# Optimization experiments

Hardware: AMD Instinct MI355X
Metric: run time of the kernel (lower is better)

## Reference

```python
import jax, jax.numpy as jnp
import numpy as np

D_MODEL = 1024
N_HEADS = 16
D_K = D_MODEL // N_HEADS


def setup_inputs() -> dict:
    key = jax.random.key(0)
    kx, kq, kk, kv, ko = jax.random.split(key, 5)
    scale = 1.0 / np.sqrt(D_MODEL)
    return {
        "x": jax.random.normal(kx, (2, 2048, D_MODEL), dtype=jnp.float32),
        "W_Q": jax.random.normal(kq, (D_MODEL, D_MODEL), dtype=jnp.float32) * scale,
        "W_K": jax.random.normal(kk, (D_MODEL, D_MODEL), dtype=jnp.float32) * scale,
        "W_V": jax.random.normal(kv, (D_MODEL, D_MODEL), dtype=jnp.float32) * scale,
        "W_O": jax.random.normal(ko, (D_MODEL, D_MODEL), dtype=jnp.float32) * scale,
    }


def reference(x, W_Q, W_K, W_V, W_O) -> jnp.ndarray:
    B, S, _ = x.shape
    # Projections; weights stored as (d_model, d_model), applied as x @ W (Linear weight transposed convention folded into init)
    def heads(w):
        return jnp.einsum('bsd,de->bse', x, w).reshape(B, S, N_HEADS, D_K).transpose(0, 2, 1, 3)
    Q, K, V = heads(W_Q), heads(W_K), heads(W_V)  # (B,H,S,d_k)
    scores = jnp.einsum('bhqd,bhkd->bhqk', Q, K) / jnp.sqrt(jnp.asarray(D_K, x.dtype))
    causal_mask = jnp.triu(jnp.ones((S, S), dtype=bool), k=1)  # True above diagonal
    scores = jnp.where(causal_mask[None, None], jnp.asarray(-jnp.inf, x.dtype), scores)
    attn = jax.nn.softmax(scores, axis=-1)
    out = jnp.einsum('bhqk,bhkd->bhqd', attn, V)  # (B,H,S,d_k)
    out = out.transpose(0, 2, 1, 3).reshape(B, S, N_HEADS * D_K)
    return jnp.einsum('bsd,de->bse', out, W_O)
```

## Files before the change

### kernel.cpp

```cpp
#include <hip/hip_runtime.h>

typedef unsigned short u16;
typedef unsigned int u32;
typedef __attribute__((ext_vector_type(8))) __bf16 bf16x8;
typedef __attribute__((ext_vector_type(2))) __bf16 bf16x2;
typedef __attribute__((ext_vector_type(4))) float f32x4;
typedef __attribute__((ext_vector_type(16))) float f32x16;
typedef __attribute__((ext_vector_type(4))) u32 u32x4;

__device__ inline u16 f2bf(float f) {
  unsigned u = __builtin_bit_cast(unsigned, f);
  u += 0x7FFFu + ((u >> 16) & 1u);
  return (u16)(u >> 16);
}

__device__ inline u32 packbf(float a, float b) {
  bf16x2 t;
  t[0] = (__bf16)a;
  t[1] = (__bf16)b;
  return __builtin_bit_cast(u32, t);
}

__device__ inline void async16(const void* g, void* l) {
  __builtin_amdgcn_global_load_lds((const __attribute__((address_space(1))) void*)g,
                                   (__attribute__((address_space(3))) void*)l, 16, 0, 0);
}

__global__ __launch_bounds__(256) void xconv(const float* __restrict__ x, u16* __restrict__ xb) {
  int i = blockIdx.x * 256 + threadIdx.x;
  float4 v = ((const float4*)x)[i];
  ushort4 r;
  r.x = f2bf(v.x); r.y = f2bf(v.y); r.z = f2bf(v.z); r.w = f2bf(v.w);
  ((ushort4*)xb)[i] = r;
}

__global__ __launch_bounds__(256) void wtrans4(const float* __restrict__ W0,
                                               const float* __restrict__ W1,
                                               const float* __restrict__ W2,
                                               const float* __restrict__ W3,
                                               u16* __restrict__ WtQKV,
                                               u16* __restrict__ WtO) {
  __shared__ u16 tile[32][33];
  const int z = blockIdx.z;
  const float* W = (z == 0) ? W0 : (z == 1) ? W1 : (z == 2) ? W2 : W3;
  u16* Wt = (z < 3) ? (WtQKV + (size_t)z * 1024 * 1024) : WtO;
  const float s = (z == 0) ? 0.18033688011112042f : 1.0f;
  const int e0 = blockIdx.x * 32;
  const int d0 = blockIdx.y * 32;
  const int tx = threadIdx.x & 31;
  const int ty = threadIdx.x >> 5;
#pragma unroll
  for (int i = ty; i < 32; i += 8)
    tile[i][tx] = f2bf(W[(size_t)(d0 + i) * 1024 + e0 + tx] * s);
  __syncthreads();
#pragma unroll
  for (int i = ty; i < 32; i += 8)
    Wt[(size_t)(e0 + i) * 1024 + d0 + tx] = tile[tx][i];
}

__global__ __launch_bounds__(256) void vtrans(const u16* __restrict__ QKV, u16* __restrict__ Vtg) {
  __shared__ u16 t[32][66];
  const int tid = threadIdx.x;
  const int s0 = blockIdx.x * 32, dg0 = blockIdx.y * 64, b = blockIdx.z;
  {
    const int i = tid >> 3, c = (tid & 7) * 8;
    uint4 v = *(const uint4*)(QKV + (size_t)(b * 2048 + s0 + i) * 3072 + 2048 + dg0 + c);
    u16 tmp[8];
    *(uint4*)tmp = v;
#pragma unroll
    for (int e = 0; e < 8; ++e) t[i][c + e] = tmp[e];
  }
  __syncthreads();
  {
    const int r = tid >> 2, cg = (tid & 3) * 8;
    u16 tmp[8];
#pragma unroll
    for (int e = 0; e < 8; ++e) tmp[e] = t[cg + e][r];
    *(uint4*)(Vtg + (size_t)(b * 1024 + dg0 + r) * 2048 + s0 + cg) = *(uint4*)tmp;
  }
}

template <int OUT_BF16>
__global__ __launch_bounds__(256) void gemm_bt(const u16* __restrict__ A,
                                               const u16* __restrict__ Bt,
                                               void* __restrict__ Cp,
                                               int M, int N, int K) {
  __shared__ __align__(16) u16 As[128 * 32];
  __shared__ __align__(16) u16 Bs[128 * 32];
  const int tid = threadIdx.x;
  const int lane = tid & 63;
  const int wave = tid >> 6;
  const int lr = lane & 15;
  const int lk = (lane >> 4) * 8;
  const int wm = (wave >> 1) * 64;
  const int wn = (wave & 1) * 64;
  const int bm = blockIdx.x * 128;
  const int bn = blockIdx.y * 128;
  const int srow = lane >> 2;
  const int scol = (lane & 3) * 8;

  f32x4 acc[4][4] = {};

  for (int k0 = 0; k0 < K; k0 += 32) {
#pragma unroll
    for (int r = 0; r < 2; ++r) {
      const int chunk = r * 4 + wave;
      const int row = chunk * 16 + srow;
      async16(A + (size_t)(bm + row) * K + k0 + scol, &As[chunk * 512 + lane * 8]);
      async16(Bt + (size_t)(bn + row) * K + k0 + scol, &Bs[chunk * 512 + lane * 8]);
    }
    __syncthreads();
    bf16x8 a[4], b[4];
#pragma unroll
    for (int i = 0; i < 4; ++i) {
      a[i] = *(const bf16x8*)&As[(wm + i * 16 + lr) * 32 + lk];
      b[i] = *(const bf16x8*)&Bs[(wn + i * 16 + lr) * 32 + lk];
    }
#pragma unroll
    for (int mi = 0; mi < 4; ++mi)
#pragma unroll
      for (int ni = 0; ni < 4; ++ni)
        acc[mi][ni] = __builtin_amdgcn_mfma_f32_16x16x32_bf16(a[mi], b[ni], acc[mi][ni], 0, 0, 0);
    __syncthreads();
  }

#pragma unroll
  for (int mi = 0; mi < 4; ++mi) {
#pragma unroll
    for (int ni = 0; ni < 4; ++ni) {
      const int col = bn + wn + ni * 16 + lr;
#pragma unroll
      for (int j = 0; j < 4; ++j) {
        const int row = bm + wm + mi * 16 + (lane >> 4) * 4 + j;
        if (OUT_BF16)
          ((u16*)Cp)[(size_t)row * N + col] = f2bf(acc[mi][ni][j]);
        else
          ((float*)Cp)[(size_t)row * N + col] = acc[mi][ni][j];
      }
    }
  }
}

__global__ __launch_bounds__(512) void attn_kernel(const u16* __restrict__ QKV,
                                                   const u16* __restrict__ Vtg,
                                                   u16* __restrict__ Opart,
                                                   float* __restrict__ Lpart) {
  constexpr int S = 2048, LD = 3072;
  constexpr float MFIX = 12.0f;
  __shared__ __align__(16) u16 Ks[2][64 * 64];
  __shared__ __align__(16) u16 Vs[2][64 * 64];

  const int g = 7 - (blockIdx.x >> 1);
  const int c = blockIdx.x & 1;
  const int bh = blockIdx.y;
  const int b = bh >> 4, h = bh & 15;
  const int tid = threadIdx.x, lane = tid & 63, w = tid >> 6;
  const int l31 = lane & 31, lh = lane >> 5;

  const int qbase = g * 256 + w * 32;
  const int ktlast = 4 * g + (w >> 1);
  const int ktbeg = c * (2 * g + 2);
  const int ktend = (c + 1) * (2 * g + 2);

  const u16* qrow = QKV + (size_t)(b * S + qbase + l31) * LD + h * 64;
  bf16x8 qf[4];
#pragma unroll
  for (int cc = 0; cc < 4; ++cc) qf[cc] = *(const bf16x8*)(qrow + cc * 16 + lh * 8);

  const int r0 = tid >> 3, x0 = ((tid & 7) ^ (r0 & 7)) << 3;
  const u16* Kbase = QKV + (size_t)b * S * LD + 1024 + h * 64;
  const u16* Vbase = Vtg + (size_t)bh * 64 * 2048;

#define STAGE(buf, kt_)                                                          \
  do {                                                                           \
    async16(Kbase + (size_t)((kt_)*64 + r0) * LD + x0, &Ks[buf][tid * 8]);       \
    async16(Vbase + (size_t)r0 * 2048 + (kt_)*64 + x0, &Vs[buf][tid * 8]);       \
  } while (0)

  f32x16 o0 = {}, o1 = {};
  float l_run = 0.f;

  STAGE(0, ktbeg);
  __syncthreads();

  int cur = 0;
  for (int kt = ktbeg; kt < ktend; ++kt) {
    if (kt + 1 < ktend) STAGE(cur ^ 1, kt + 1);

    const bool active = (kt <= ktlast);
    const bool hiA = active && ((kt < ktlast) || (w & 1));

    if (active) {
      const u16* ks = Ks[cur];
      const u16* vs = Vs[cur];

      f32x16 t0 = {}, t1 = {};
      __builtin_amdgcn_s_setprio(1);
#pragma unroll
      for (int cc = 0; cc < 4; ++cc) {
        const int ci = 2 * cc + lh;
        const bf16x8 kf0 = *(const bf16x8*)&ks[l31 * 64 + ((ci ^ (l31 & 7)) << 3)];
        t0 = __builtin_amdgcn_mfma_f32_32x32x16_bf16(kf0, qf[cc], t0, 0, 0, 0);
        if (hiA) {
          const bf16x8 kf1 = *(const bf16x8*)&ks[(32 + l31) * 64 + ((ci ^ (l31 & 7)) << 3)];
          t1 = __builtin_amdgcn_mfma_f32_32x32x16_bf16(kf1, qf[cc], t1, 0, 0, 0);
        }
      }
      __builtin_amdgcn_s_setprio(0);

      if (kt == ktlast) {
        const int kb = kt * 64 + 4 * lh;
        const int qa = qbase + l31;
#pragma unroll
        for (int r = 0; r < 16; ++r) {
          const int ko = (r & 3) + 8 * (r >> 2);
          if (kb + ko > qa) t0[r] = -3e38f;
          if (hiA && (kb + 32 + ko > qa)) t1[r] = -3e38f;
        }
      }

      f32x16 p0 = t0, p1 = t1;
#pragma unroll
      for (int r = 0; r < 16; ++r) p0[r] = exp2f(t0[r] - MFIX);
      if (hiA) {
#pragma unroll
        for (int r = 0; r < 16; ++r) p1[r] = exp2f(t1[r] - MFIX);
      }
      float v[16];
#pragma unroll
      for (int r = 0; r < 16; ++r) v[r] = hiA ? (p0[r] + p1[r]) : p0[r];
#pragma unroll
      for (int s = 8; s >= 1; s >>= 1)
#pragma unroll
        for (int r = 0; r < s; ++r) v[r] += v[r + s];
      l_run += v[0];

      u32 pk0[8], pk1[8], sw0[8], sw1[8];
#pragma unroll
      for (int j = 0; j < 8; ++j) pk0[j] = packbf(p0[2 * j], p0[2 * j + 1]);
#pragma unroll
      for (int j = 0; j < 8; ++j) sw0[j] = __shfl_xor(pk0[j], 32);
      if (hiA) {
#pragma unroll
        for (int j = 0; j < 8; ++j) pk1[j] = packbf(p1[2 * j], p1[2 * j + 1]);
#pragma unroll
        for (int j = 0; j < 8; ++j) sw1[j] = __shfl_xor(pk1[j], 32);
      }

      __builtin_amdgcn_s_setprio(1);
#define PVSTEP(kc, pk, sw)                                                             \
      {                                                                                \
        const int q4 = ((kc) & 1) * 4;                                                 \
        u32x4 wv;                                                                      \
        wv[0] = lh ? sw[q4 + 2] : pk[q4 + 0];                                          \
        wv[1] = lh ? sw[q4 + 3] : pk[q4 + 1];                                          \
        wv[2] = lh ? pk[q4 + 2] : sw[q4 + 0];                                          \
        wv[3] = lh ? pk[q4 + 3] : sw[q4 + 1];                                          \
        const bf16x8 pa = __builtin_bit_cast(bf16x8, wv);                              \
        const int ci = 2 * (kc) + lh;                                                  \
        const bf16x8 vf0 = *(const bf16x8*)&vs[l31 * 64 + ((ci ^ (l31 & 7)) << 3)];    \
        const bf16x8 vf1 = *(const bf16x8*)&vs[(32 + l31) * 64 + ((ci ^ (l31 & 7)) << 3)]; \
        o0 = __builtin_amdgcn_mfma_f32_32x32x16_bf16(pa, vf0, o0, 0, 0, 0);            \
        o1 = __builtin_amdgcn_mfma_f32_32x32x16_bf16(pa, vf1, o1, 0, 0, 0);            \
      }
      PVSTEP(0, pk0, sw0)
      PVSTEP(1, pk0, sw0)
      if (hiA) {
        PVSTEP(2, pk1, sw1)
        PVSTEP(3, pk1, sw1)
      }
#undef PVSTEP
      __builtin_amdgcn_s_setprio(0);
    }

    __syncthreads();
    cur ^= 1;
  }
#undef STAGE

  u16* Oc = Opart + (size_t)c * 4096 * 1024;
#pragma unroll
  for (int r = 0; r < 16; ++r) {
    const int qo = (r & 3) + 8 * (r >> 2) + 4 * lh;
    u16* op = Oc + (size_t)(b * S + qbase + qo) * 1024 + h * 64 + l31;
    op[0] = f2bf(o0[r]);
    op[32] = f2bf(o1[r]);
  }
  const float l_tot = l_run + __shfl_xor(l_run, 32);
  if (lh == 0)
    Lpart[(size_t)c * 4096 * 16 + (size_t)(b * S + qbase + l31) * 16 + h] = l_tot;
}

__global__ __launch_bounds__(256) void combine(const u16* __restrict__ Opart,
                                               const float* __restrict__ Lpart,
                                               u16* __restrict__ Obuf) {
  const int i = blockIdx.x * 256 + threadIdx.x;
  const int row = i >> 7;
  const int cw = (i & 127) * 8;
  const int h = cw >> 6;
  const float l = Lpart[(size_t)row * 16 + h] + Lpart[(size_t)4096 * 16 + (size_t)row * 16 + h];
  const float inv = 1.0f / l;
  const bf16x8 a = *(const bf16x8*)(Opart + (size_t)row * 1024 + cw);
  const bf16x8 bq = *(const bf16x8*)(Opart + (size_t)4096 * 1024 + (size_t)row * 1024 + cw);
  u16 out[8];
#pragma unroll
  for (int j = 0; j < 8; ++j) out[j] = f2bf(((float)a[j] + (float)bq[j]) * inv);
  *(uint4*)(Obuf + (size_t)row * 1024 + cw) = *(uint4*)out;
}

extern "C" void kernel_launch(void* const* d_in, const int* in_sizes, int n_in,
                              void* d_out, int out_size, void* d_ws, size_t ws_size,
                              hipStream_t stream) {
  const float* x  = (const float*)d_in[0];
  const float* WQ = (const float*)d_in[1];
  const float* WK = (const float*)d_in[2];
  const float* WV = (const float*)d_in[3];
  const float* WO = (const float*)d_in[4];
  float* out = (float*)d_out;

  u16* xb    = (u16*)d_ws;
  u16* WtQKV = xb + (size_t)4096 * 1024;
  u16* WtO   = WtQKV + (size_t)3072 * 1024;
  u16* QKV   = WtO + (size_t)1024 * 1024;
  u16* Obuf  = QKV + (size_t)4096 * 3072;
  u16* Vtg   = Obuf + (size_t)4096 * 1024;
  u16* Opart = Vtg + (size_t)2048 * 2048;
  float* Lpart = (float*)(Opart + (size_t)2 * 4096 * 1024);

  xconv<<<4096, 256, 0, stream>>>(x, xb);
  wtrans4<<<dim3(32, 32, 4), 256, 0, stream>>>(WQ, WK, WV, WO, WtQKV, WtO);

  gemm_bt<1><<<dim3(32, 24), 256, 0, stream>>>(xb, WtQKV, QKV, 4096, 3072, 1024);
  vtrans<<<dim3(64, 16, 2), 256, 0, stream>>>(QKV, Vtg);
  attn_kernel<<<dim3(16, 32), 512, 0, stream>>>(QKV, Vtg, Opart, Lpart);
  combine<<<2048, 256, 0, stream>>>(Opart, Lpart, Obuf);
  gemm_bt<0><<<dim3(32, 8), 256, 0, stream>>>(Obuf, WtO, out, 4096, 1024, 1024);
}
```

Baseline: 165.5 us.

## Drop LDS staging and KV split in attention, load K/V tiles directly to registers

Attention is restructured. The two-way key split and its combine kernel are removed. Each 256-thread block now covers 128 query rows, and blocks are ordered heaviest-first and interleaved across heads. K and V fragments are loaded straight from global memory into registers with software prefetch of the next tile, and the LDS double buffer and barriers are gone. Normalization is folded into the output write, which saves one launch and the partial-output traffic, but it loses K/V sharing across waves through LDS, so every wave re-reads K/V from global memory or cache.

```diff
diff --git a/kernel.cpp b/kernel.cpp
--- a/kernel.cpp
+++ b/kernel.cpp
@@ -141,171 +141,153 @@
   }
 }
 
-__global__ __launch_bounds__(512) void attn_kernel(const u16* __restrict__ QKV,
+__global__ __launch_bounds__(256) void attn_kernel(const u16* __restrict__ QKV,
                                                    const u16* __restrict__ Vtg,
-                                                   u16* __restrict__ Opart,
-                                                   float* __restrict__ Lpart) {
+                                                   u16* __restrict__ Obuf) {
   constexpr int S = 2048, LD = 3072;
   constexpr float MFIX = 12.0f;
-  __shared__ __align__(16) u16 Ks[2][64 * 64];
-  __shared__ __align__(16) u16 Vs[2][64 * 64];
-
-  const int g = 7 - (blockIdx.x >> 1);
-  const int c = blockIdx.x & 1;
-  const int bh = blockIdx.y;
+
+  const int bid = blockIdx.x;
+  const int r8 = bid & 7;
+  const int s = bid >> 3;
+  const int bh = r8 * 4 + (s >> 4);
+  const int g = 15 - (s & 15);
   const int b = bh >> 4, h = bh & 15;
   const int tid = threadIdx.x, lane = tid & 63, w = tid >> 6;
   const int l31 = lane & 31, lh = lane >> 5;
 
-  const int qbase = g * 256 + w * 32;
-  const int ktlast = 4 * g + (w >> 1);
-  const int ktbeg = c * (2 * g + 2);
-  const int ktend = (c + 1) * (2 * g + 2);
+  const int qbase = g * 128 + w * 32;
+  const int ktlast = qbase >> 6;
+  const int nkt = ktlast + 1;
 
   const u16* qrow = QKV + (size_t)(b * S + qbase + l31) * LD + h * 64;
   bf16x8 qf[4];
 #pragma unroll
   for (int cc = 0; cc < 4; ++cc) qf[cc] = *(const bf16x8*)(qrow + cc * 16 + lh * 8);
 
-  const int r0 = tid >> 3, x0 = ((tid & 7) ^ (r0 & 7)) << 3;
-  const u16* Kbase = QKV + (size_t)b * S * LD + 1024 + h * 64;
-  const u16* Vbase = Vtg + (size_t)bh * 64 * 2048;
-
-#define STAGE(buf, kt_)                                                          \
-  do {                                                                           \
-    async16(Kbase + (size_t)((kt_)*64 + r0) * LD + x0, &Ks[buf][tid * 8]);       \
-    async16(Vbase + (size_t)r0 * 2048 + (kt_)*64 + x0, &Vs[buf][tid * 8]);       \
+  const u16* Krow0 = QKV + (size_t)(b * S + l31) * LD + 1024 + h * 64;
+  const u16* Krow1 = Krow0 + (size_t)32 * LD;
+  const u16* Vrow0 = Vtg + (size_t)(bh * 64 + l31) * 2048;
+  const u16* Vrow1 = Vtg + (size_t)(bh * 64 + 32 + l31) * 2048;
+
+  bf16x8 kf0[4], kf1[4], vf0[4], vf1[4];
+
+#define LOADK(kt_)                                                                   \
+  do {                                                                               \
+    const u16* p0 = Krow0 + (size_t)(kt_) * 64 * LD;                                 \
+    const u16* p1 = Krow1 + (size_t)(kt_) * 64 * LD;                                 \
+    _Pragma("unroll") for (int cc = 0; cc < 4; ++cc) {                               \
+      kf0[cc] = *(const bf16x8*)(p0 + cc * 16 + lh * 8);                             \
+      kf1[cc] = *(const bf16x8*)(p1 + cc * 16 + lh * 8);                             \
+    }                                                                                \
+  } while (0)
+
+#define LOADV(kt_)                                                                   \
+  do {                                                                               \
+    const u16* p0 = Vrow0 + (kt_) * 64;                                              \
+    const u16* p1 = Vrow1 + (kt_) * 64;                                              \
+    _Pragma("unroll") for (int cc = 0; cc < 4; ++cc) {                               \
+      vf0[cc] = *(const bf16x8*)(p0 + cc * 16 + lh * 8);                             \
+      vf1[cc] = *(const bf16x8*)(p1 + cc * 16 + lh * 8);                             \
+    }                                                                                \
   } while (0)
 
   f32x16 o0 = {}, o1 = {};
   float l_run = 0.f;
 
-  STAGE(0, ktbeg);
-  __syncthreads();
-
-  int cur = 0;
-  for (int kt = ktbeg; kt < ktend; ++kt) {
-    if (kt + 1 < ktend) STAGE(cur ^ 1, kt + 1);
-
-    const bool active = (kt <= ktlast);
-    const bool hiA = active && ((kt < ktlast) || (w & 1));
-
-    if (active) {
-      const u16* ks = Ks[cur];
-      const u16* vs = Vs[cur];
-
-      f32x16 t0 = {}, t1 = {};
-      __builtin_amdgcn_s_setprio(1);
-#pragma unroll
-      for (int cc = 0; cc < 4; ++cc) {
-        const int ci = 2 * cc + lh;
-        const bf16x8 kf0 = *(const bf16x8*)&ks[l31 * 64 + ((ci ^ (l31 & 7)) << 3)];
-        t0 = __builtin_amdgcn_mfma_f32_32x32x16_bf16(kf0, qf[cc], t0, 0, 0, 0);
-        if (hiA) {
-          const bf16x8 kf1 = *(const bf16x8*)&ks[(32 + l31) * 64 + ((ci ^ (l31 & 7)) << 3)];
-          t1 = __builtin_amdgcn_mfma_f32_32x32x16_bf16(kf1, qf[cc], t1, 0, 0, 0);
-        }
+  LOADK(0);
+  LOADV(0);
+
+  for (int kt = 0; kt < nkt; ++kt) {
+    const bool hi = (kt < ktlast) || (w & 1);
+
+    f32x16 t0 = {}, t1 = {};
+    __builtin_amdgcn_s_setprio(1);
+#pragma unroll
+    for (int cc = 0; cc < 4; ++cc) {
+      t0 = __builtin_amdgcn_mfma_f32_32x32x16_bf16(kf0[cc], qf[cc], t0, 0, 0, 0);
+      if (hi) t1 = __builtin_amdgcn_mfma_f32_32x32x16_bf16(kf1[cc], qf[cc], t1, 0, 0, 0);
+    }
+    __builtin_amdgcn_s_setprio(0);
+
+    if (kt + 1 < nkt) LOADK(kt + 1);
+
+    if (kt == ktlast) {
+      const int kb = kt * 64 + 4 * lh;
+      const int qa = qbase + l31;
+#pragma unroll
+      for (int r = 0; r < 16; ++r) {
+        const int ko = (r & 3) + 8 * (r >> 2);
+        if (kb + ko > qa) t0[r] = -3e38f;
+        if (hi && (kb + 32 + ko > qa)) t1[r] = -3e38f;
       }
-      __builtin_amdgcn_s_setprio(0);
-
-      if (kt == ktlast) {
-        const int kb = kt * 64 + 4 * lh;
-        const int qa = qbase + l31;
-#pragma unroll
-        for (int r = 0; r < 16; ++r) {
-          const int ko = (r & 3) + 8 * (r >> 2);
-          if (kb + ko > qa) t0[r] = -3e38f;
-          if (hiA && (kb + 32 + ko > qa)) t1[r] = -3e38f;
-        }
-      }
-
-      f32x16 p0 = t0, p1 = t1;
-#pragma unroll
-      for (int r = 0; r < 16; ++r) p0[r] = exp2f(t0[r] - MFIX);
-      if (hiA) {
-#pragma unroll
-        for (int r = 0; r < 16; ++r) p1[r] = exp2f(t1[r] - MFIX);
-      }
-      float v[16];
-#pragma unroll
-      for (int r = 0; r < 16; ++r) v[r] = hiA ? (p0[r] + p1[r]) : p0[r];
-#pragma unroll
-      for (int s = 8; s >= 1; s >>= 1)
-#pragma unroll
-        for (int r = 0; r < s; ++r) v[r] += v[r + s];
-      l_run += v[0];
-
-      u32 pk0[8], pk1[8], sw0[8], sw1[8];
-#pragma unroll
-      for (int j = 0; j < 8; ++j) pk0[j] = packbf(p0[2 * j], p0[2 * j + 1]);
-#pragma unroll
-      for (int j = 0; j < 8; ++j) sw0[j] = __shfl_xor(pk0[j], 32);
-      if (hiA) {
-#pragma unroll
-        for (int j = 0; j < 8; ++j) pk1[j] = packbf(p1[2 * j], p1[2 * j + 1]);
-#pragma unroll
-        for (int j = 0; j < 8; ++j) sw1[j] = __shfl_xor(pk1[j], 32);
-      }
-
-      __builtin_amdgcn_s_setprio(1);
-#define PVSTEP(kc, pk, sw)                                                             \
-      {                                                                                \
-        const int q4 = ((kc) & 1) * 4;                                                 \
-        u32x4 wv;                                                                      \
-        wv[0] = lh ? sw[q4 + 2] : pk[q4 + 0];                                          \
-        wv[1] = lh ? sw[q4 + 3] : pk[q4 + 1];                                          \
-        wv[2] = lh ? pk[q4 + 2] : sw[q4 + 0];                                          \
-        wv[3] = lh ? pk[q4 + 3] : sw[q4 + 1];                                          \
-        const bf16x8 pa = __builtin_bit_cast(bf16x8, wv);                              \
-        const int ci = 2 * (kc) + lh;                                                  \
-        const bf16x8 vf0 = *(const bf16x8*)&vs[l31 * 64 + ((ci ^ (l31 & 7)) << 3)];    \
-        const bf16x8 vf1 = *(const bf16x8*)&vs[(32 + l31) * 64 + ((ci ^ (l31 & 7)) << 3)]; \
-        o0 = __builtin_amdgcn_mfma_f32_32x32x16_bf16(pa, vf0, o0, 0, 0, 0);            \
-        o1 = __builtin_amdgcn_mfma_f32_32x32x16_bf16(pa, vf1, o1, 0, 0, 0);            \
-      }
-      PVSTEP(0, pk0, sw0)
-      PVSTEP(1, pk0, sw0)
-      if (hiA) {
-        PVSTEP(2, pk1, sw1)
-        PVSTEP(3, pk1, sw1)
-      }
+    }
+
+    f32x16 p0 = t0, p1 = t1;
+#pragma unroll
+    for (int r = 0; r < 16; ++r) p0[r] = exp2f(t0[r] - MFIX);
+    if (hi) {
+#pragma unroll
+      for (int r = 0; r < 16; ++r) p1[r] = exp2f(t1[r] - MFIX);
+    }
+    float v[16];
+#pragma unroll
+    for (int r = 0; r < 16; ++r) v[r] = hi ? (p0[r] + p1[r]) : p0[r];
+#pragma unroll
+    for (int ss = 8; ss >= 1; ss >>= 1)
+#pragma unroll
+      for (int r = 0; r < ss; ++r) v[r] += v[r + ss];
+    l_run += v[0];
+
+    u32 pk0[8], pk1[8], sw0[8], sw1[8];
+#pragma unroll
+    for (int j = 0; j < 8; ++j) pk0[j] = packbf(p0[2 * j], p0[2 * j + 1]);
+#pragma unroll
+    for (int j = 0; j < 8; ++j) sw0[j] = __shfl_xor(pk0[j], 32);
+    if (hi) {
+#pragma unroll
+      for (int j = 0; j < 8; ++j) pk1[j] = packbf(p1[2 * j], p1[2 * j + 1]);
+#pragma unroll
+      for (int j = 0; j < 8; ++j) sw1[j] = __shfl_xor(pk1[j], 32);
+    }
+
+    __builtin_amdgcn_s_setprio(1);
+#define PVSTEP(kc, pk, sw)                                                           \
+    {                                                                                \
+      const int q4 = ((kc) & 1) * 4;                                                 \
+      u32x4 wv;                                                                      \
+      wv[0] = lh ? sw[q4 + 2] : pk[q4 + 0];                                          \
+      wv[1] = lh ? sw[q4 + 3] : pk[q4 + 1];                                          \
+      wv[2] = lh ? pk[q4 + 2] : sw[q4 + 0];                                          \
+      wv[3] = lh ? pk[q4 + 3] : sw[q4 + 1];                                          \
+      const bf16x8 pa = __builtin_bit_cast(bf16x8, wv);                              \
+      o0 = __builtin_amdgcn_mfma_f32_32x32x16_bf16(pa, vf0[kc], o0, 0, 0, 0);        \
+      o1 = __builtin_amdgcn_mfma_f32_32x32x16_bf16(pa, vf1[kc], o1, 0, 0, 0);        \
+    }
+    PVSTEP(0, pk0, sw0)
+    PVSTEP(1, pk0, sw0)
+    if (hi) {
+      PVSTEP(2, pk1, sw1)
+      PVSTEP(3, pk1, sw1)
+    }
 #undef PVSTEP
-      __builtin_amdgcn_s_setprio(0);
-    }
-
-    __syncthreads();
-    cur ^= 1;
-  }
-#undef STAGE
-
-  u16* Oc = Opart + (size_t)c * 4096 * 1024;
+    __builtin_amdgcn_s_setprio(0);
+
+    if (kt + 1 < nkt) LOADV(kt + 1);
+  }
+#undef LOADK
+#undef LOADV
+
+  const float l_tot = l_run + __shfl_xor(l_run, 32);
+  const float linv = 1.0f / l_tot;
 #pragma unroll
   for (int r = 0; r < 16; ++r) {
     const int qo = (r & 3) + 8 * (r >> 2) + 4 * lh;
-    u16* op = Oc + (size_t)(b * S + qbase + qo) * 1024 + h * 64 + l31;
-    op[0] = f2bf(o0[r]);
-    op[32] = f2bf(o1[r]);
-  }
-  const float l_tot = l_run + __shfl_xor(l_run, 32);
-  if (lh == 0)
-    Lpart[(size_t)c * 4096 * 16 + (size_t)(b * S + qbase + l31) * 16 + h] = l_tot;
-}
-
-__global__ __launch_bounds__(256) void combine(const u16* __restrict__ Opart,
-                                               const float* __restrict__ Lpart,
-                                               u16* __restrict__ Obuf) {
-  const int i = blockIdx.x * 256 + threadIdx.x;
-  const int row = i >> 7;
-  const int cw = (i & 127) * 8;
-  const int h = cw >> 6;
-  const float l = Lpart[(size_t)row * 16 + h] + Lpart[(size_t)4096 * 16 + (size_t)row * 16 + h];
-  const float inv = 1.0f / l;
-  const bf16x8 a = *(const bf16x8*)(Opart + (size_t)row * 1024 + cw);
-  const bf16x8 bq = *(const bf16x8*)(Opart + (size_t)4096 * 1024 + (size_t)row * 1024 + cw);
-  u16 out[8];
-#pragma unroll
-  for (int j = 0; j < 8; ++j) out[j] = f2bf(((float)a[j] + (float)bq[j]) * inv);
-  *(uint4*)(Obuf + (size_t)row * 1024 + cw) = *(uint4*)out;
+    const float lq = __shfl(linv, qo);
+    u16* op = Obuf + (size_t)(b * S + qbase + qo) * 1024 + h * 64 + l31;
+    op[0] = f2bf(o0[r] * lq);
+    op[32] = f2bf(o1[r] * lq);
+  }
 }
 
 extern "C" void kernel_launch(void* const* d_in, const int* in_sizes, int n_in,
@@ -324,15 +306,12 @@
   u16* QKV   = WtO + (size_t)1024 * 1024;
   u16* Obuf  = QKV + (size_t)4096 * 3072;
   u16* Vtg   = Obuf + (size_t)4096 * 1024;
-  u16* Opart = Vtg + (size_t)2048 * 2048;
-  float* Lpart = (float*)(Opart + (size_t)2 * 4096 * 1024);
 
   xconv<<<4096, 256, 0, stream>>>(x, xb);
   wtrans4<<<dim3(32, 32, 4), 256, 0, stream>>>(WQ, WK, WV, WO, WtQKV, WtO);
 
   gemm_bt<1><<<dim3(32, 24), 256, 0, stream>>>(xb, WtQKV, QKV, 4096, 3072, 1024);
   vtrans<<<dim3(64, 16, 2), 256, 0, stream>>>(QKV, Vtg);
-  attn_kernel<<<dim3(16, 32), 512, 0, stream>>>(QKV, Vtg, Opart, Lpart);
-  combine<<<2048, 256, 0, stream>>>(Opart, Lpart, Obuf);
+  attn_kernel<<<512, 256, 0, stream>>>(QKV, Vtg, Obuf);
   gemm_bt<0><<<dim3(32, 8), 256, 0, stream>>>(Obuf, WtO, out, 4096, 1024, 1024);
 }
```

Result: slower. 197.1 us (+19.1%).
